# Optimization experiments

Hardware: AMD Instinct MI355X
Metric: run time of the kernel (lower is better)

Reference implementation:

```python
import jax, jax.numpy as jnp
import numpy as np

K_SIZE = 5  # local window size (odd, SAME padding, stride 1)


def _local_attn(x_main, x_ref, W_main, W_ref, k_size=K_SIZE):
    # 1x1 convs == per-pixel channel matmuls
    cm = jnp.einsum('bhwc,cd->bhwd', x_main, W_main)  # query  [B,H,W,C']
    cr = jnp.einsum('bhwc,cd->bhwd', x_ref, W_ref)    # keys   [B,H,W,C']
    pad = (k_size - 1) // 2
    B, H, W, C = cr.shape
    crp = jnp.pad(cr, ((0, 0), (pad, pad), (pad, pad), (0, 0)))
    # score for each of the k*k offsets: dot(query, shifted key) per pixel.
    # Avoids materializing the [B,H,W,k*k,C] patch tensor.
    scores = [
        jnp.einsum('bhwc,bhwc->bhw', cm, crp[:, i:i + H, j:j + W, :])
        for i in range(k_size) for j in range(k_size)
    ]
    # the layer concatenates the query itself as the last "key" (self score)
    scores.append(jnp.einsum('bhwc,bhwc->bhw', cm, cm))
    attn = jnp.stack(scores, axis=-1)  # [B,H,W,k*k+1]
    return jax.nn.softmax(attn, axis=-1)


def setup_inputs() -> dict:
    key = jax.random.key(0)
    k1, k2, k3, k4 = jax.random.split(key, 4)
    B, H, W, C = 4, 128, 128, 64
    Ci = 64  # intermediate_dim
    return {
        'x_main': jax.random.normal(k1, (B, H, W, C), jnp.float32),
        'x_ref': jax.random.normal(k2, (B, H, W, C), jnp.float32),
        'W_main': jax.random.normal(k3, (C, Ci), jnp.float32) * (2.0 / C) ** 0.5,
        'W_ref': jax.random.normal(k4, (C, Ci), jnp.float32) * (2.0 / C) ** 0.5,
    }


def reference(x_main, x_ref, W_main, W_ref):
    return _local_attn(x_main, x_ref, W_main, W_ref)
```

## Files before the change

### kernel.cpp

```cpp
#include <hip/hip_runtime.h>
#include <math.h>

#define HDIM 128
#define WDIM 128
#define CDIM 64
#define BDIM 4
#define NPIX (BDIM * HDIM * WDIM)

__global__ __launch_bounds__(256, 1)
void conv1x1_kernel(const float* __restrict__ xm,
                    const float* __restrict__ xr,
                    const float* __restrict__ Wm,
                    const float* __restrict__ Wr,
                    float* __restrict__ outm,
                    float* __restrict__ outr) {
    const float* x; const float* Wg; float* out;
    if (blockIdx.y == 0) { x = xm; Wg = Wm; out = outm; }
    else                 { x = xr; Wg = Wr; out = outr; }

    __shared__ float Ws[32][64];
    __shared__ float xs[32][260];

    const int t = threadIdx.x;
    const int pxbase = blockIdx.x * 256;
    const int dg = t & 7;
    const int pg = t >> 3;

    float acc[8][8];
    #pragma unroll
    for (int i = 0; i < 8; ++i)
        #pragma unroll
        for (int j = 0; j < 8; ++j) acc[i][j] = 0.f;

    for (int kc = 0; kc < 2; ++kc) {
        {
            const float4* Wg4 = (const float4*)(Wg + kc * 32 * CDIM);
            float4* Ws4 = (float4*)&Ws[0][0];
            Ws4[t]       = Wg4[t];
            Ws4[t + 256] = Wg4[t + 256];
        }
        #pragma unroll
        for (int i = 0; i < 8; ++i) {
            int L  = t + 256 * i;
            int px = L >> 3;
            int c4 = L & 7;
            float4 v = *(const float4*)&x[(size_t)(pxbase + px) * CDIM
                                          + kc * 32 + 4 * c4];
            int ppx = px ^ (8 * (c4 & 3));
            xs[4 * c4 + 0][ppx] = v.x;
            xs[4 * c4 + 1][ppx] = v.y;
            xs[4 * c4 + 2][ppx] = v.z;
            xs[4 * c4 + 3][ppx] = v.w;
        }
        __syncthreads();

        #pragma unroll 4
        for (int c = 0; c < 32; ++c) {
            const int s = (c >> 2) & 3;
            const float4* xp = (const float4*)&xs[c][8 * (pg ^ s)];
            const float4* wp = (const float4*)&Ws[c][8 * dg];
            float4 x0 = xp[0], x1 = xp[1];
            float4 w0 = wp[0], w1 = wp[1];
            float xa[8] = {x0.x, x0.y, x0.z, x0.w, x1.x, x1.y, x1.z, x1.w};
            float wa[8] = {w0.x, w0.y, w0.z, w0.w, w1.x, w1.y, w1.z, w1.w};
            #pragma unroll
            for (int i = 0; i < 8; ++i)
                #pragma unroll
                for (int j = 0; j < 8; ++j)
                    acc[i][j] = fmaf(xa[i], wa[j], acc[i][j]);
        }
        __syncthreads();
    }

    #pragma unroll
    for (int i = 0; i < 8; ++i) {
        int px = pxbase + pg * 8 + i;
        float4 o0 = {acc[i][0], acc[i][1], acc[i][2], acc[i][3]};
        float4 o1 = {acc[i][4], acc[i][5], acc[i][6], acc[i][7]};
        *(float4*)&out[(size_t)px * CDIM + dg * 8]     = o0;
        *(float4*)&out[(size_t)px * CDIM + dg * 8 + 4] = o1;
    }
}

#define TILE_W 16
#define TILE_H 8
#define HALO_W 20
#define HALO_H 12
#define NHALO (HALO_W * HALO_H)
#define PSTRIDE 68

__global__ __launch_bounds__(256, 1)
void attn_tiled_kernel(const float* __restrict__ cm,
                       const float* __restrict__ cr,
                       float* __restrict__ out) {
    __shared__ float crs[NHALO * PSTRIDE];

    const int t   = threadIdx.x;
    const int tx0 = blockIdx.x * TILE_W;
    const int ty0 = blockIdx.y * TILE_H;
    const int b   = blockIdx.z;

    #pragma unroll
    for (int it = 0; it < 15; ++it) {
        int L   = t + 256 * it;
        int pix = L >> 4;
        int q   = L & 15;
        int hy  = pix / HALO_W;
        int hx  = pix - hy * HALO_W;
        int gy  = ty0 + hy - 2, gx = tx0 + hx - 2;
        float4 v = make_float4(0.f, 0.f, 0.f, 0.f);
        if (gy >= 0 && gy < HDIM && gx >= 0 && gx < WDIM) {
            size_t gp = ((size_t)b * HDIM + gy) * WDIM + gx;
            v = *(const float4*)&cr[gp * CDIM + 4 * q];
        }
        *(float4*)&crs[pix * PSTRIDE + 4 * q] = v;
    }
    __syncthreads();

    const int pl = t >> 1;
    const int cg = t & 1;
    const int lx = pl & (TILE_W - 1);
    const int ly = pl >> 4;
    const size_t gpx = ((size_t)b * HDIM + ty0 + ly) * WDIM + tx0 + lx;

    float4 qv[8];
    {
        const float4* cmp = (const float4*)&cm[gpx * CDIM + cg * 32];
        #pragma unroll
        for (int m = 0; m < 8; ++m) qv[m] = cmp[m];
    }

    float s[26];
    #pragma unroll
    for (int k = 0; k < 25; ++k) {
        const int i = k / 5, j = k % 5;
        const int p = (ly + i) * HALO_W + (lx + j);
        const float4* kp = (const float4*)&crs[p * PSTRIDE + cg * 32];
        float acc = 0.f;
        #pragma unroll
        for (int m = 0; m < 8; ++m) {
            float4 v = kp[m];
            acc = fmaf(qv[m].x, v.x, acc);
            acc = fmaf(qv[m].y, v.y, acc);
            acc = fmaf(qv[m].z, v.z, acc);
            acc = fmaf(qv[m].w, v.w, acc);
        }
        s[k] = acc;
    }
    {
        float acc = 0.f;
        #pragma unroll
        for (int m = 0; m < 8; ++m) {
            float4 v = qv[m];
            acc = fmaf(v.x, v.x, acc);
            acc = fmaf(v.y, v.y, acc);
            acc = fmaf(v.z, v.z, acc);
            acc = fmaf(v.w, v.w, acc);
        }
        s[25] = acc;
    }

    #pragma unroll
    for (int k = 0; k < 26; ++k) s[k] += __shfl_xor(s[k], 1);

    float mx = s[0];
    #pragma unroll
    for (int k = 1; k < 26; ++k) mx = fmaxf(mx, s[k]);
    float sum = 0.f;
    #pragma unroll
    for (int k = 0; k < 26; ++k) { s[k] = __expf(s[k] - mx); sum += s[k]; }
    const float inv = 1.f / sum;

    float* op = &out[gpx * 26 + cg * 13];
    if (cg == 0) {
        #pragma unroll
        for (int k = 0; k < 13; ++k) op[k] = s[k] * inv;
    } else {
        #pragma unroll
        for (int k = 0; k < 13; ++k) op[k] = s[13 + k] * inv;
    }
}

extern "C" void kernel_launch(void* const* d_in, const int* in_sizes, int n_in,
                              void* d_out, int out_size, void* d_ws, size_t ws_size,
                              hipStream_t stream) {
    const float* xm = (const float*)d_in[0];
    const float* xr = (const float*)d_in[1];
    const float* Wm = (const float*)d_in[2];
    const float* Wr = (const float*)d_in[3];
    float* outp = (float*)d_out;

    float* cm = (float*)d_ws;
    float* cr = cm + (size_t)NPIX * CDIM;

    dim3 g1(NPIX / 256, 2);
    conv1x1_kernel<<<g1, 256, 0, stream>>>(xm, xr, Wm, Wr, cm, cr);

    dim3 g2(WDIM / TILE_W, HDIM / TILE_H, BDIM);
    attn_tiled_kernel<<<g2, 256, 0, stream>>>(cm, cr, outp);
}
```

Before: 107.7 us.

## Fuse 1x1 projections into the tiled local attention kernel

Merges the conv1x1 projection kernel and the attention kernel into one kernel per 16x8 tile. The query projection is computed for the tile and the key projection for its 20x12 halo, both in registers, then staged through shared memory for the 25-offset dot products and softmax. This removes the global write and re-read of the intermediate cm/cr tensors and one launch. In exchange, key projections are recomputed for halo pixels (240 vs 128 per tile), and each block now does more serial work under high register pressure.

Result: faster. 102.9 us (-4.4%).

```diff
diff --git a/kernel.cpp b/kernel.cpp
--- a/kernel.cpp
+++ b/kernel.cpp
@@ -7,58 +7,116 @@
 #define BDIM 4
 #define NPIX (BDIM * HDIM * WDIM)
 
+#define TILE_W 16
+#define TILE_H 8
+#define HALO_W 20
+#define HALO_H 12
+#define NHALO (HALO_W * HALO_H)
+#define MSLOT 256
+#define PSTRIDE 68
+#define XSTRIDE 260
+
 __global__ __launch_bounds__(256, 1)
-void conv1x1_kernel(const float* __restrict__ xm,
-                    const float* __restrict__ xr,
-                    const float* __restrict__ Wm,
-                    const float* __restrict__ Wr,
-                    float* __restrict__ outm,
-                    float* __restrict__ outr) {
-    const float* x; const float* Wg; float* out;
-    if (blockIdx.y == 0) { x = xm; Wg = Wm; out = outm; }
-    else                 { x = xr; Wg = Wr; out = outr; }
-
-    __shared__ float Ws[32][64];
-    __shared__ float xs[32][260];
-
-    const int t = threadIdx.x;
-    const int pxbase = blockIdx.x * 256;
+void fused_local_attn_kernel(const float* __restrict__ xm,
+                             const float* __restrict__ xr,
+                             const float* __restrict__ Wm,
+                             const float* __restrict__ Wr,
+                             float* __restrict__ out) {
+    __shared__ float lds[16320];
+    float* Wsh = lds;
+    float* xsh = lds + 2048;
+
+    const int t   = threadIdx.x;
+    const int tx0 = blockIdx.x * TILE_W;
+    const int ty0 = blockIdx.y * TILE_H;
+    const int b   = blockIdx.z;
+
     const int dg = t & 7;
     const int pg = t >> 3;
 
-    float acc[8][8];
-    #pragma unroll
-    for (int i = 0; i < 8; ++i)
-        #pragma unroll
-        for (int j = 0; j < 8; ++j) acc[i][j] = 0.f;
+    float cmv[4][8];
+    #pragma unroll
+    for (int i = 0; i < 4; ++i)
+        #pragma unroll
+        for (int j = 0; j < 8; ++j) cmv[i][j] = 0.f;
 
     for (int kc = 0; kc < 2; ++kc) {
         {
-            const float4* Wg4 = (const float4*)(Wg + kc * 32 * CDIM);
-            float4* Ws4 = (float4*)&Ws[0][0];
-            Ws4[t]       = Wg4[t];
-            Ws4[t + 256] = Wg4[t + 256];
-        }
-        #pragma unroll
-        for (int i = 0; i < 8; ++i) {
+            const float4* Wg4 = (const float4*)(Wm + kc * 32 * CDIM);
+            ((float4*)Wsh)[t]       = Wg4[t];
+            ((float4*)Wsh)[t + 256] = Wg4[t + 256];
+        }
+        #pragma unroll
+        for (int i = 0; i < 4; ++i) {
             int L  = t + 256 * i;
             int px = L >> 3;
             int c4 = L & 7;
-            float4 v = *(const float4*)&x[(size_t)(pxbase + px) * CDIM
-                                          + kc * 32 + 4 * c4];
+            size_t gp = ((size_t)b * HDIM + ty0 + (px >> 4)) * WDIM
+                        + tx0 + (px & 15);
+            float4 v = *(const float4*)&xm[gp * CDIM + kc * 32 + 4 * c4];
             int ppx = px ^ (8 * (c4 & 3));
-            xs[4 * c4 + 0][ppx] = v.x;
-            xs[4 * c4 + 1][ppx] = v.y;
-            xs[4 * c4 + 2][ppx] = v.z;
-            xs[4 * c4 + 3][ppx] = v.w;
-        }
-        __syncthreads();
-
+            xsh[(4 * c4 + 0) * XSTRIDE + ppx] = v.x;
+            xsh[(4 * c4 + 1) * XSTRIDE + ppx] = v.y;
+            xsh[(4 * c4 + 2) * XSTRIDE + ppx] = v.z;
+            xsh[(4 * c4 + 3) * XSTRIDE + ppx] = v.w;
+        }
+        __syncthreads();
         #pragma unroll 4
         for (int c = 0; c < 32; ++c) {
             const int s = (c >> 2) & 3;
-            const float4* xp = (const float4*)&xs[c][8 * (pg ^ s)];
-            const float4* wp = (const float4*)&Ws[c][8 * dg];
+            float4 xv = *(const float4*)&xsh[c * XSTRIDE + ((4 * pg) ^ (8 * s))];
+            const float4* wp = (const float4*)&Wsh[c * 64 + 8 * dg];
+            float4 w0 = wp[0], w1 = wp[1];
+            float xa[4] = {xv.x, xv.y, xv.z, xv.w};
+            float wa[8] = {w0.x, w0.y, w0.z, w0.w, w1.x, w1.y, w1.z, w1.w};
+            #pragma unroll
+            for (int i = 0; i < 4; ++i)
+                #pragma unroll
+                for (int j = 0; j < 8; ++j)
+                    cmv[i][j] = fmaf(xa[i], wa[j], cmv[i][j]);
+        }
+        __syncthreads();
+    }
+
+    float crv[8][8];
+    #pragma unroll
+    for (int i = 0; i < 8; ++i)
+        #pragma unroll
+        for (int j = 0; j < 8; ++j) crv[i][j] = 0.f;
+
+    for (int kc = 0; kc < 2; ++kc) {
+        {
+            const float4* Wg4 = (const float4*)(Wr + kc * 32 * CDIM);
+            ((float4*)Wsh)[t]       = Wg4[t];
+            ((float4*)Wsh)[t + 256] = Wg4[t + 256];
+        }
+        #pragma unroll
+        for (int i = 0; i < 8; ++i) {
+            int L    = t + 256 * i;
+            int slot = L >> 3;
+            int c4   = L & 7;
+            float4 v = make_float4(0.f, 0.f, 0.f, 0.f);
+            if (slot < NHALO) {
+                int hy = slot / HALO_W;
+                int hx = slot - hy * HALO_W;
+                int gy = ty0 + hy - 2, gx = tx0 + hx - 2;
+                if (gy >= 0 && gy < HDIM && gx >= 0 && gx < WDIM) {
+                    size_t gp = ((size_t)b * HDIM + gy) * WDIM + gx;
+                    v = *(const float4*)&xr[gp * CDIM + kc * 32 + 4 * c4];
+                }
+            }
+            int ppx = slot ^ (8 * (c4 & 3));
+            xsh[(4 * c4 + 0) * XSTRIDE + ppx] = v.x;
+            xsh[(4 * c4 + 1) * XSTRIDE + ppx] = v.y;
+            xsh[(4 * c4 + 2) * XSTRIDE + ppx] = v.z;
+            xsh[(4 * c4 + 3) * XSTRIDE + ppx] = v.w;
+        }
+        __syncthreads();
+        #pragma unroll 4
+        for (int c = 0; c < 32; ++c) {
+            const int s = (c >> 2) & 3;
+            const float4* xp = (const float4*)&xsh[c * XSTRIDE + ((8 * pg) ^ (8 * s))];
+            const float4* wp = (const float4*)&Wsh[c * 64 + 8 * dg];
             float4 x0 = xp[0], x1 = xp[1];
             float4 w0 = wp[0], w1 = wp[1];
             float xa[8] = {x0.x, x0.y, x0.z, x0.w, x1.x, x1.y, x1.z, x1.w};
@@ -67,75 +125,51 @@
             for (int i = 0; i < 8; ++i)
                 #pragma unroll
                 for (int j = 0; j < 8; ++j)
-                    acc[i][j] = fmaf(xa[i], wa[j], acc[i][j]);
-        }
-        __syncthreads();
-    }
-
-    #pragma unroll
-    for (int i = 0; i < 8; ++i) {
-        int px = pxbase + pg * 8 + i;
-        float4 o0 = {acc[i][0], acc[i][1], acc[i][2], acc[i][3]};
-        float4 o1 = {acc[i][4], acc[i][5], acc[i][6], acc[i][7]};
-        *(float4*)&out[(size_t)px * CDIM + dg * 8]     = o0;
-        *(float4*)&out[(size_t)px * CDIM + dg * 8 + 4] = o1;
-    }
-}
-
-#define TILE_W 16
-#define TILE_H 8
-#define HALO_W 20
-#define HALO_H 12
-#define NHALO (HALO_W * HALO_H)
-#define PSTRIDE 68
-
-__global__ __launch_bounds__(256, 1)
-void attn_tiled_kernel(const float* __restrict__ cm,
-                       const float* __restrict__ cr,
-                       float* __restrict__ out) {
-    __shared__ float crs[NHALO * PSTRIDE];
-
-    const int t   = threadIdx.x;
-    const int tx0 = blockIdx.x * TILE_W;
-    const int ty0 = blockIdx.y * TILE_H;
-    const int b   = blockIdx.z;
-
-    #pragma unroll
-    for (int it = 0; it < 15; ++it) {
-        int L   = t + 256 * it;
-        int pix = L >> 4;
-        int q   = L & 15;
-        int hy  = pix / HALO_W;
-        int hx  = pix - hy * HALO_W;
-        int gy  = ty0 + hy - 2, gx = tx0 + hx - 2;
-        float4 v = make_float4(0.f, 0.f, 0.f, 0.f);
-        if (gy >= 0 && gy < HDIM && gx >= 0 && gx < WDIM) {
-            size_t gp = ((size_t)b * HDIM + gy) * WDIM + gx;
-            v = *(const float4*)&cr[gp * CDIM + 4 * q];
-        }
-        *(float4*)&crs[pix * PSTRIDE + 4 * q] = v;
+                    crv[i][j] = fmaf(xa[i], wa[j], crv[i][j]);
+        }
+        __syncthreads();
+    }
+
+    #pragma unroll
+    for (int i = 0; i < 4; ++i) {
+        int px = 4 * pg + i;
+        float4 o0 = {cmv[i][0], cmv[i][1], cmv[i][2], cmv[i][3]};
+        float4 o1 = {cmv[i][4], cmv[i][5], cmv[i][6], cmv[i][7]};
+        *(float4*)&lds[px * PSTRIDE + 8 * dg]     = o0;
+        *(float4*)&lds[px * PSTRIDE + 8 * dg + 4] = o1;
     }
     __syncthreads();
 
     const int pl = t >> 1;
     const int cg = t & 1;
+    float4 qv[8];
+    #pragma unroll
+    for (int m = 0; m < 8; ++m)
+        qv[m] = *(const float4*)&lds[pl * PSTRIDE + cg * 32 + 4 * m];
+    __syncthreads();
+
+    #pragma unroll
+    for (int i = 0; i < 8; ++i) {
+        int slot = 8 * pg + i;
+        if (slot < NHALO) {
+            float4 o0 = {crv[i][0], crv[i][1], crv[i][2], crv[i][3]};
+            float4 o1 = {crv[i][4], crv[i][5], crv[i][6], crv[i][7]};
+            *(float4*)&lds[slot * PSTRIDE + 8 * dg]     = o0;
+            *(float4*)&lds[slot * PSTRIDE + 8 * dg + 4] = o1;
+        }
+    }
+    __syncthreads();
+
     const int lx = pl & (TILE_W - 1);
     const int ly = pl >> 4;
     const size_t gpx = ((size_t)b * HDIM + ty0 + ly) * WDIM + tx0 + lx;
 
-    float4 qv[8];
-    {
-        const float4* cmp = (const float4*)&cm[gpx * CDIM + cg * 32];
-        #pragma unroll
-        for (int m = 0; m < 8; ++m) qv[m] = cmp[m];
-    }
-
     float s[26];
     #pragma unroll
     for (int k = 0; k < 25; ++k) {
         const int i = k / 5, j = k % 5;
         const int p = (ly + i) * HALO_W + (lx + j);
-        const float4* kp = (const float4*)&crs[p * PSTRIDE + cg * 32];
+        const float4* kp = (const float4*)&lds[p * PSTRIDE + cg * 32];
         float acc = 0.f;
         #pragma unroll
         for (int m = 0; m < 8; ++m) {
@@ -190,12 +224,6 @@
     const float* Wr = (const float*)d_in[3];
     float* outp = (float*)d_out;
 
-    float* cm = (float*)d_ws;
-    float* cr = cm + (size_t)NPIX * CDIM;
-
-    dim3 g1(NPIX / 256, 2);
-    conv1x1_kernel<<<g1, 256, 0, stream>>>(xm, xr, Wm, Wr, cm, cr);
-
-    dim3 g2(WDIM / TILE_W, HDIM / TILE_H, BDIM);
-    attn_tiled_kernel<<<g2, 256, 0, stream>>>(cm, cr, outp);
+    dim3 g(WDIM / TILE_W, HDIM / TILE_H, BDIM);
+    fused_local_attn_kernel<<<g, 256, 0, stream>>>(xm, xr, Wm, Wr, outp);
 }
```
